# Performance work log

Hardware: AMD Instinct MI355X
Metric: run time of the kernel (lower is better)

Reference implementation:

```python
import jax, jax.numpy as jnp
import numpy as np

N_NODES = 50000


def setup_inputs() -> dict:
    key = jax.random.key(0)
    k1, k2, k3, k4 = jax.random.split(key, 4)
    in_c, hid = 256, 128
    x = jax.random.normal(k1, (N_NODES, in_c), dtype=jnp.float32)
    edge_index = jax.random.randint(k2, (2, 800000), 0, N_NODES, dtype=jnp.int32)
    # GCNConv weight (glorot) and bias
    W_conv = jax.random.normal(k3, (in_c, hid), dtype=jnp.float32) * (1.0 / np.sqrt(in_c))
    b_conv = jnp.zeros((hid,), dtype=jnp.float32)
    # Final Linear (xavier_uniform per reset_parameters)
    limit = np.sqrt(6.0 / (hid + in_c))
    W_lin = jax.random.uniform(k4, (hid, in_c), dtype=jnp.float32, minval=-limit, maxval=limit)
    b_lin = jnp.zeros((in_c,), dtype=jnp.float32)
    return {"x": x, "edge_index": edge_index, "W_conv": W_conv, "b_conv": b_conv,
            "W_lin": W_lin, "b_lin": b_lin}


def _gcn_conv(x, edge_index, W, b):
    n = x.shape[0]
    # add self-loops (standard GCN normalization)
    loop = jnp.arange(n, dtype=edge_index.dtype)
    src = jnp.concatenate([edge_index[0], loop])
    dst = jnp.concatenate([edge_index[1], loop])
    # transform first (in_c -> hid) so the edge gather moves the smaller dim
    h = x @ W  # [N, hid]
    deg = jax.ops.segment_sum(jnp.ones_like(dst, dtype=h.dtype), dst, num_segments=n)
    dinv = jnp.where(deg > 0, jax.lax.rsqrt(deg), 0.0)
    norm = dinv[src] * dinv[dst]  # [E+N]
    msg = h[src] * norm[:, None]  # [E+N, hid]
    out = jax.ops.segment_sum(msg, dst, num_segments=n)
    return out + b


def reference(x, edge_index, W_conv, b_conv, W_lin, b_lin):
    h = _gcn_conv(x, edge_index, W_conv, b_conv)  # [N, hid]
    # dropout p=0.0 -> identity
    return h @ W_lin + b_lin  # [N, in_c]
```

## Files before the change

kernel.cpp:

```cpp
#include <hip/hip_runtime.h>
#include <hip/hip_fp16.h>


#define N_NODES 50000
#define N_EDGES 800000
#define IN_C 256
#define HID 128
#define SCAN_BLOCKS ((N_NODES + 255) / 256)
#define GEMM_MBLK ((N_NODES + 63) / 64)

#define OFF_H    0UL
#define OFF_CONV 12800000UL
#define OFF_DEG  25600000UL
#define OFF_RP   25800000UL
#define OFF_DINV 26000064UL
#define OFF_RANK 26200064UL
#define OFF_REC  27800064UL
#define OFF_BSUM 31000064UL
#define OFF_WT1  31001088UL
#define OFF_WT2  31066624UL

typedef __attribute__((ext_vector_type(8))) short bf16x8;
typedef __attribute__((ext_vector_type(4))) float f32x4;

__device__ __forceinline__ ushort f2bf(float x) {
    unsigned u = __float_as_uint(x);
    u += 0x7fffu + ((u >> 16) & 1u);
    return (ushort)(u >> 16);
}

__global__ void deg_kernel(const int* __restrict__ dst, int* __restrict__ deg,
                           ushort* __restrict__ rank, int e) {
    int i = blockIdx.x * blockDim.x + threadIdx.x;
    if (i < e) rank[i] = (ushort)atomicAdd(&deg[dst[i]], 1);
}

__global__ __launch_bounds__(256) void scan_blocks_kernel(
    const int* __restrict__ deg, int* __restrict__ row_ptr,
    int* __restrict__ bsums, int n)
{
    __shared__ int tmp[256];
    int tid = threadIdx.x;
    int i = blockIdx.x * 256 + tid;
    int v = (i < n) ? deg[i] : 0;
    int orig = v;
    tmp[tid] = v;
    __syncthreads();
    #pragma unroll
    for (int off = 1; off < 256; off <<= 1) {
        int t = (tid >= off) ? tmp[tid - off] : 0;
        __syncthreads();
        tmp[tid] += t;
        __syncthreads();
    }
    if (i < n) row_ptr[i] = tmp[tid] - orig;
    if (tid == 255) bsums[blockIdx.x] = tmp[255];
}

__global__ __launch_bounds__(256) void scan_sums_kernel(int* __restrict__ bsums, int nb) {
    __shared__ int tmp[256];
    int tid = threadIdx.x;
    int v = (tid < nb) ? bsums[tid] : 0;
    int orig = v;
    tmp[tid] = v;
    __syncthreads();
    #pragma unroll
    for (int off = 1; off < 256; off <<= 1) {
        int t = (tid >= off) ? tmp[tid - off] : 0;
        __syncthreads();
        tmp[tid] += t;
        __syncthreads();
    }
    if (tid < nb) bsums[tid] = tmp[tid] - orig;
}

__global__ __launch_bounds__(256) void finalize_kernel(
    const int* __restrict__ deg, int* __restrict__ row_ptr,
    const int* __restrict__ bsums, float* __restrict__ dinv, int n)
{
    int i = blockIdx.x * 256 + threadIdx.x;
    if (i < n) {
        row_ptr[i] += bsums[blockIdx.x];
        dinv[i] = rsqrtf((float)(deg[i] + 1));
    }
    if (i == 0) row_ptr[n] = N_EDGES;
}

#define BUCKET_BLOCKS 2048
__global__ __launch_bounds__(256) void bucket_kernel(
    const int* __restrict__ src, const int* __restrict__ dst,
    const ushort* __restrict__ rank, const int* __restrict__ row_ptr,
    const float* __restrict__ dinv, unsigned* __restrict__ rec)
{
    int cls = blockIdx.x & 7;
    int blk = blockIdx.x >> 3;
    int lo = cls * (N_NODES / 8);
    int hi = lo + (N_NODES / 8);
    const int CHUNK = (N_EDGES + 255) / 256;
    int e0 = blk * CHUNK;
    int e1 = min(e0 + CHUNK, N_EDGES);
    for (int i = e0 + threadIdx.x; i < e1; i += 256) {
        int d = dst[i];
        if (d >= lo && d < hi) {
            int s = src[i];
            unsigned r = (unsigned)(ushort)s |
                         ((unsigned)__half_as_ushort(__float2half_rn(dinv[s])) << 16);
            rec[row_ptr[d] + rank[i]] = r;
        }
    }
}

__global__ void transpose_w_kernel(const float* __restrict__ W, ushort* __restrict__ Wt,
                                   int K, int N) {
    int i = blockIdx.x * 256 + threadIdx.x;
    if (i < N * K) {
        int n = i / K, k = i % K;
        Wt[i] = f2bf(W[k * N + n]);
    }
}

template <bool A_IS_BF16, bool BF16OUT>
__global__ __launch_bounds__(256) void mfma_gemm_kernel(
    const void* __restrict__ Av, const ushort* __restrict__ Bt,
    const float* __restrict__ bias, void* __restrict__ Cv,
    int M, int N, int K)
{
    constexpr int LDK = 40;
    __shared__ ushort As[64 * LDK];
    __shared__ ushort Bs[128 * LDK];
    int tid = threadIdx.x;
    int wave = tid >> 6, lane = tid & 63;
    int quad = lane >> 4, l16 = lane & 15;
    int wm0 = (wave >> 1) * 32, wn0 = (wave & 1) * 64;
    int bm = blockIdx.x * 64, bn = blockIdx.y * 128;

    f32x4 acc[2][4] = {};

    for (int k0 = 0; k0 < K; k0 += 32) {
        {
            int row = tid >> 2, col = (tid & 3) * 8;
            int grow = bm + row;
            if (A_IS_BF16) {
                bf16x8 v = {};
                if (grow < M)
                    v = *(const bf16x8*)((const ushort*)Av + (size_t)grow * K + k0 + col);
                *(bf16x8*)&As[row * LDK + col] = v;
            } else {
                float4 v0 = make_float4(0.f, 0.f, 0.f, 0.f);
                float4 v1 = make_float4(0.f, 0.f, 0.f, 0.f);
                if (grow < M) {
                    const float* ap = (const float*)Av + (size_t)grow * K + k0 + col;
                    v0 = *(const float4*)ap;
                    v1 = *(const float4*)(ap + 4);
                }
                ushort t[8] = {f2bf(v0.x), f2bf(v0.y), f2bf(v0.z), f2bf(v0.w),
                               f2bf(v1.x), f2bf(v1.y), f2bf(v1.z), f2bf(v1.w)};
                *(bf16x8*)&As[row * LDK + col] = *(bf16x8*)t;
            }
        }
        {
            int ch = tid * 2;
            int n = ch >> 2;
            int kk = (ch & 3) * 8;
            const ushort* bp = Bt + (size_t)(bn + n) * K + k0 + kk;
            *(bf16x8*)&Bs[n * LDK + kk]     = *(const bf16x8*)bp;
            *(bf16x8*)&Bs[n * LDK + kk + 8] = *(const bf16x8*)(bp + 8);
        }
        __syncthreads();
        bf16x8 af[2], bfr[4];
        #pragma unroll
        for (int im = 0; im < 2; ++im)
            af[im] = *(bf16x8*)&As[(wm0 + im * 16 + l16) * LDK + quad * 8];
        #pragma unroll
        for (int in = 0; in < 4; ++in)
            bfr[in] = *(bf16x8*)&Bs[(wn0 + in * 16 + l16) * LDK + quad * 8];
        #pragma unroll
        for (int im = 0; im < 2; ++im)
            #pragma unroll
            for (int in = 0; in < 4; ++in)
                acc[im][in] = __builtin_amdgcn_mfma_f32_16x16x32_bf16(
                    af[im], bfr[in], acc[im][in], 0, 0, 0);
        __syncthreads();
    }
    #pragma unroll
    for (int im = 0; im < 2; ++im) {
        #pragma unroll
        for (int in = 0; in < 4; ++in) {
            int col = bn + wn0 + in * 16 + l16;
            float bval = bias ? bias[col] : 0.f;
            #pragma unroll
            for (int r = 0; r < 4; ++r) {
                int grow = bm + wm0 + im * 16 + quad * 4 + r;
                if (grow < M) {
                    float o = acc[im][in][r] + bval;
                    if (BF16OUT)
                        ((ushort*)Cv)[(size_t)grow * N + col] = f2bf(o);
                    else
                        ((float*)Cv)[(size_t)grow * N + col] = o;
                }
            }
        }
    }
}

__global__ __launch_bounds__(256) void gather_kernel(
    const ushort* __restrict__ hb, const int* __restrict__ row_ptr,
    const unsigned* __restrict__ rec, const float* __restrict__ dinv,
    const float* __restrict__ b_conv, ushort* __restrict__ convb, int n)
{
    int wave = threadIdx.x >> 6;
    int lane = threadIdx.x & 63;
    int d = blockIdx.x * 4 + wave;
    if (d >= n) return;
    int c = lane << 1;
    float di = dinv[d];
    unsigned hv = *(const unsigned*)&hb[(size_t)d * HID + c];
    float2 acc;
    acc.x = di * __uint_as_float(hv << 16);
    acc.y = di * __uint_as_float(hv & 0xffff0000u);
    int begin = row_ptr[d], end = row_ptr[d + 1];
    int e = begin;
    for (; e + 4 <= end; e += 4) {
        unsigned r0 = rec[e], r1 = rec[e + 1], r2 = rec[e + 2], r3 = rec[e + 3];
        unsigned s0 = r0 & 0xffffu, s1 = r1 & 0xffffu, s2 = r2 & 0xffffu, s3 = r3 & 0xffffu;
        float w0 = __half2float(__ushort_as_half((ushort)(r0 >> 16)));
        float w1 = __half2float(__ushort_as_half((ushort)(r1 >> 16)));
        float w2 = __half2float(__ushort_as_half((ushort)(r2 >> 16)));
        float w3 = __half2float(__ushort_as_half((ushort)(r3 >> 16)));
        unsigned v0 = *(const unsigned*)&hb[(size_t)s0 * HID + c];
        unsigned v1 = *(const unsigned*)&hb[(size_t)s1 * HID + c];
        unsigned v2 = *(const unsigned*)&hb[(size_t)s2 * HID + c];
        unsigned v3 = *(const unsigned*)&hb[(size_t)s3 * HID + c];
        acc.x += w0 * __uint_as_float(v0 << 16);
        acc.y += w0 * __uint_as_float(v0 & 0xffff0000u);
        acc.x += w1 * __uint_as_float(v1 << 16);
        acc.y += w1 * __uint_as_float(v1 & 0xffff0000u);
        acc.x += w2 * __uint_as_float(v2 << 16);
        acc.y += w2 * __uint_as_float(v2 & 0xffff0000u);
        acc.x += w3 * __uint_as_float(v3 << 16);
        acc.y += w3 * __uint_as_float(v3 & 0xffff0000u);
    }
    for (; e < end; ++e) {
        unsigned r0 = rec[e];
        unsigned s0 = r0 & 0xffffu;
        float w0 = __half2float(__ushort_as_half((ushort)(r0 >> 16)));
        unsigned v0 = *(const unsigned*)&hb[(size_t)s0 * HID + c];
        acc.x += w0 * __uint_as_float(v0 << 16);
        acc.y += w0 * __uint_as_float(v0 & 0xffff0000u);
    }
    float ox = di * acc.x + b_conv[c];
    float oy = di * acc.y + b_conv[c + 1];
    unsigned po = ((unsigned)f2bf(oy) << 16) | (unsigned)f2bf(ox);
    *(unsigned*)&convb[(size_t)d * HID + c] = po;
}

extern "C" void kernel_launch(void* const* d_in, const int* in_sizes, int n_in,
                              void* d_out, int out_size, void* d_ws, size_t ws_size,
                              hipStream_t stream) {
    const float* x      = (const float*)d_in[0];
    const int*   ei     = (const int*)d_in[1];
    const float* W_conv = (const float*)d_in[2];
    const float* b_conv = (const float*)d_in[3];
    const float* W_lin  = (const float*)d_in[4];
    const float* b_lin  = (const float*)d_in[5];
    float* out = (float*)d_out;

    char* ws = (char*)d_ws;
    ushort* hb      = (ushort*)(ws + OFF_H);
    ushort* convb   = (ushort*)(ws + OFF_CONV);
    int*    deg     = (int*)(ws + OFF_DEG);
    int*    row_ptr = (int*)(ws + OFF_RP);
    float*  dinv    = (float*)(ws + OFF_DINV);
    ushort* rank    = (ushort*)(ws + OFF_RANK);
    unsigned* rec   = (unsigned*)(ws + OFF_REC);
    int*    bsums   = (int*)(ws + OFF_BSUM);
    ushort* wt_conv = (ushort*)(ws + OFF_WT1);
    ushort* wt_lin  = (ushort*)(ws + OFF_WT2);

    const int* src = ei;
    const int* dst = ei + N_EDGES;

    hipMemsetAsync(deg, 0, 200000, stream);

    deg_kernel<<<(N_EDGES + 255) / 256, 256, 0, stream>>>(dst, deg, rank, N_EDGES);
    scan_blocks_kernel<<<SCAN_BLOCKS, 256, 0, stream>>>(deg, row_ptr, bsums, N_NODES);
    scan_sums_kernel<<<1, 256, 0, stream>>>(bsums, SCAN_BLOCKS);
    finalize_kernel<<<SCAN_BLOCKS, 256, 0, stream>>>(deg, row_ptr, bsums, dinv, N_NODES);
    bucket_kernel<<<BUCKET_BLOCKS, 256, 0, stream>>>(src, dst, rank, row_ptr, dinv, rec);

    transpose_w_kernel<<<(HID * IN_C + 255) / 256, 256, 0, stream>>>(W_conv, wt_conv, IN_C, HID);
    transpose_w_kernel<<<(IN_C * HID + 255) / 256, 256, 0, stream>>>(W_lin, wt_lin, HID, IN_C);

    mfma_gemm_kernel<false, true><<<dim3(GEMM_MBLK, HID / 128), 256, 0, stream>>>(
        x, wt_conv, nullptr, hb, N_NODES, HID, IN_C);

    gather_kernel<<<(N_NODES + 3) / 4, 256, 0, stream>>>(
        hb, row_ptr, rec, dinv, b_conv, convb, N_NODES);

    mfma_gemm_kernel<true, false><<<dim3(GEMM_MBLK, IN_C / 128), 256, 0, stream>>>(
        convb, wt_lin, b_lin, out, N_NODES, IN_C, HID);
}
```

Before: 238.8 us.

## Vectorize gather, shrink rank to bytes, fuse scan and transpose launches

```diff
diff --git a/kernel.cpp b/kernel.cpp
--- a/kernel.cpp
+++ b/kernel.cpp
@@ -15,13 +15,14 @@
 #define OFF_RP   25800000UL
 #define OFF_DINV 26000064UL
 #define OFF_RANK 26200064UL
-#define OFF_REC  27800064UL
-#define OFF_BSUM 31000064UL
-#define OFF_WT1  31001088UL
-#define OFF_WT2  31066624UL
+#define OFF_REC  27000064UL
+#define OFF_BSUM 30200064UL
+#define OFF_WT1  30201088UL
+#define OFF_WT2  30266624UL
 
 typedef __attribute__((ext_vector_type(8))) short bf16x8;
 typedef __attribute__((ext_vector_type(4))) float f32x4;
+typedef unsigned char uchar;
 
 __device__ __forceinline__ ushort f2bf(float x) {
     unsigned u = __float_as_uint(x);
@@ -30,9 +31,9 @@
 }
 
 __global__ void deg_kernel(const int* __restrict__ dst, int* __restrict__ deg,
-                           ushort* __restrict__ rank, int e) {
+                           uchar* __restrict__ rank, int e) {
     int i = blockIdx.x * blockDim.x + threadIdx.x;
-    if (i < e) rank[i] = (ushort)atomicAdd(&deg[dst[i]], 1);
+    if (i < e) rank[i] = (uchar)atomicAdd(&deg[dst[i]], 1);
 }
 
 __global__ __launch_bounds__(256) void scan_blocks_kernel(
@@ -57,65 +58,68 @@
     if (tid == 255) bsums[blockIdx.x] = tmp[255];
 }
 
-__global__ __launch_bounds__(256) void scan_sums_kernel(int* __restrict__ bsums, int nb) {
-    __shared__ int tmp[256];
+__global__ __launch_bounds__(256) void finalize_kernel(
+    const int* __restrict__ deg, int* __restrict__ row_ptr,
+    const int* __restrict__ bsums, float* __restrict__ dinv, int n, int nb)
+{
+    __shared__ int red[256];
     int tid = threadIdx.x;
-    int v = (tid < nb) ? bsums[tid] : 0;
-    int orig = v;
-    tmp[tid] = v;
+    red[tid] = (tid < nb && tid < (int)blockIdx.x) ? bsums[tid] : 0;
     __syncthreads();
     #pragma unroll
-    for (int off = 1; off < 256; off <<= 1) {
-        int t = (tid >= off) ? tmp[tid - off] : 0;
-        __syncthreads();
-        tmp[tid] += t;
-        __syncthreads();
-    }
-    if (tid < nb) bsums[tid] = tmp[tid] - orig;
-}
-
-__global__ __launch_bounds__(256) void finalize_kernel(
-    const int* __restrict__ deg, int* __restrict__ row_ptr,
-    const int* __restrict__ bsums, float* __restrict__ dinv, int n)
-{
-    int i = blockIdx.x * 256 + threadIdx.x;
+    for (int off = 128; off > 0; off >>= 1) {
+        if (tid < off) red[tid] += red[tid + off];
+        __syncthreads();
+    }
+    int offset = red[0];
+    int i = blockIdx.x * 256 + tid;
     if (i < n) {
-        row_ptr[i] += bsums[blockIdx.x];
+        row_ptr[i] += offset;
         dinv[i] = rsqrtf((float)(deg[i] + 1));
     }
     if (i == 0) row_ptr[n] = N_EDGES;
 }
 
 #define BUCKET_BLOCKS 2048
+#define BUCKET_CHUNK 3128
 __global__ __launch_bounds__(256) void bucket_kernel(
     const int* __restrict__ src, const int* __restrict__ dst,
-    const ushort* __restrict__ rank, const int* __restrict__ row_ptr,
+    const uchar* __restrict__ rank, const int* __restrict__ row_ptr,
     const float* __restrict__ dinv, unsigned* __restrict__ rec)
 {
     int cls = blockIdx.x & 7;
     int blk = blockIdx.x >> 3;
     int lo = cls * (N_NODES / 8);
     int hi = lo + (N_NODES / 8);
-    const int CHUNK = (N_EDGES + 255) / 256;
-    int e0 = blk * CHUNK;
-    int e1 = min(e0 + CHUNK, N_EDGES);
-    for (int i = e0 + threadIdx.x; i < e1; i += 256) {
-        int d = dst[i];
-        if (d >= lo && d < hi) {
-            int s = src[i];
-            unsigned r = (unsigned)(ushort)s |
-                         ((unsigned)__half_as_ushort(__float2half_rn(dinv[s])) << 16);
-            rec[row_ptr[d] + rank[i]] = r;
+    int e0 = blk * BUCKET_CHUNK;
+    int e1 = min(e0 + BUCKET_CHUNK, N_EDGES);
+    for (int i = e0 + threadIdx.x * 4; i < e1; i += 1024) {
+        int4 d4 = *(const int4*)&dst[i];
+        #pragma unroll
+        for (int k = 0; k < 4; ++k) {
+            int d = (k == 0) ? d4.x : (k == 1) ? d4.y : (k == 2) ? d4.z : d4.w;
+            if (d >= lo && d < hi) {
+                int s = src[i + k];
+                unsigned r = (unsigned)(ushort)s |
+                             ((unsigned)__half_as_ushort(__float2half_rn(dinv[s])) << 16);
+                rec[row_ptr[d] + rank[i + k]] = r;
+            }
         }
     }
 }
 
-__global__ void transpose_w_kernel(const float* __restrict__ W, ushort* __restrict__ Wt,
-                                   int K, int N) {
+__global__ void transpose_w_kernel(const float* __restrict__ W_conv,
+                                   const float* __restrict__ W_lin,
+                                   ushort* __restrict__ wt_conv,
+                                   ushort* __restrict__ wt_lin) {
     int i = blockIdx.x * 256 + threadIdx.x;
-    if (i < N * K) {
-        int n = i / K, k = i % K;
-        Wt[i] = f2bf(W[k * N + n]);
+    if (i < HID * IN_C) {
+        int nn = i / IN_C, k = i % IN_C;
+        wt_conv[i] = f2bf(W_conv[k * HID + nn]);
+    } else {
+        int j = i - HID * IN_C;
+        int nn = j / HID, k = j % HID;
+        wt_lin[j] = f2bf(W_lin[k * IN_C + nn]);
     }
 }
 
@@ -203,6 +207,21 @@
     }
 }
 
+__device__ __forceinline__ void acc_edge(float4& a0, float4& a1, unsigned r,
+                                         const ushort* __restrict__ hb, int c) {
+    unsigned s = r & 0xffffu;
+    float w = __half2float(__ushort_as_half((ushort)(r >> 16)));
+    uint4 v = *(const uint4*)&hb[(size_t)s * HID + c];
+    a0.x += w * __uint_as_float(v.x << 16);
+    a0.y += w * __uint_as_float(v.x & 0xffff0000u);
+    a0.z += w * __uint_as_float(v.y << 16);
+    a0.w += w * __uint_as_float(v.y & 0xffff0000u);
+    a1.x += w * __uint_as_float(v.z << 16);
+    a1.y += w * __uint_as_float(v.z & 0xffff0000u);
+    a1.z += w * __uint_as_float(v.w << 16);
+    a1.w += w * __uint_as_float(v.w & 0xffff0000u);
+}
+
 __global__ __launch_bounds__(256) void gather_kernel(
     const ushort* __restrict__ hb, const int* __restrict__ row_ptr,
     const unsigned* __restrict__ rec, const float* __restrict__ dinv,
@@ -212,46 +231,56 @@
     int lane = threadIdx.x & 63;
     int d = blockIdx.x * 4 + wave;
     if (d >= n) return;
-    int c = lane << 1;
-    float di = dinv[d];
-    unsigned hv = *(const unsigned*)&hb[(size_t)d * HID + c];
-    float2 acc;
-    acc.x = di * __uint_as_float(hv << 16);
-    acc.y = di * __uint_as_float(hv & 0xffff0000u);
+    int grp = lane >> 4;
+    int l16 = lane & 15;
+    int c = l16 << 3;
+
+    float4 a0 = make_float4(0.f, 0.f, 0.f, 0.f);
+    float4 a1 = make_float4(0.f, 0.f, 0.f, 0.f);
     int begin = row_ptr[d], end = row_ptr[d + 1];
-    int e = begin;
-    for (; e + 4 <= end; e += 4) {
-        unsigned r0 = rec[e], r1 = rec[e + 1], r2 = rec[e + 2], r3 = rec[e + 3];
-        unsigned s0 = r0 & 0xffffu, s1 = r1 & 0xffffu, s2 = r2 & 0xffffu, s3 = r3 & 0xffffu;
-        float w0 = __half2float(__ushort_as_half((ushort)(r0 >> 16)));
-        float w1 = __half2float(__ushort_as_half((ushort)(r1 >> 16)));
-        float w2 = __half2float(__ushort_as_half((ushort)(r2 >> 16)));
-        float w3 = __half2float(__ushort_as_half((ushort)(r3 >> 16)));
-        unsigned v0 = *(const unsigned*)&hb[(size_t)s0 * HID + c];
-        unsigned v1 = *(const unsigned*)&hb[(size_t)s1 * HID + c];
-        unsigned v2 = *(const unsigned*)&hb[(size_t)s2 * HID + c];
-        unsigned v3 = *(const unsigned*)&hb[(size_t)s3 * HID + c];
-        acc.x += w0 * __uint_as_float(v0 << 16);
-        acc.y += w0 * __uint_as_float(v0 & 0xffff0000u);
-        acc.x += w1 * __uint_as_float(v1 << 16);
-        acc.y += w1 * __uint_as_float(v1 & 0xffff0000u);
-        acc.x += w2 * __uint_as_float(v2 << 16);
-        acc.y += w2 * __uint_as_float(v2 & 0xffff0000u);
-        acc.x += w3 * __uint_as_float(v3 << 16);
-        acc.y += w3 * __uint_as_float(v3 & 0xffff0000u);
-    }
-    for (; e < end; ++e) {
+    int e = begin + grp;
+    for (; e + 12 < end; e += 16) {
         unsigned r0 = rec[e];
-        unsigned s0 = r0 & 0xffffu;
-        float w0 = __half2float(__ushort_as_half((ushort)(r0 >> 16)));
-        unsigned v0 = *(const unsigned*)&hb[(size_t)s0 * HID + c];
-        acc.x += w0 * __uint_as_float(v0 << 16);
-        acc.y += w0 * __uint_as_float(v0 & 0xffff0000u);
-    }
-    float ox = di * acc.x + b_conv[c];
-    float oy = di * acc.y + b_conv[c + 1];
-    unsigned po = ((unsigned)f2bf(oy) << 16) | (unsigned)f2bf(ox);
-    *(unsigned*)&convb[(size_t)d * HID + c] = po;
+        unsigned r1 = rec[e + 4];
+        unsigned r2 = rec[e + 8];
+        unsigned r3 = rec[e + 12];
+        acc_edge(a0, a1, r0, hb, c);
+        acc_edge(a0, a1, r1, hb, c);
+        acc_edge(a0, a1, r2, hb, c);
+        acc_edge(a0, a1, r3, hb, c);
+    }
+    for (; e < end; e += 4)
+        acc_edge(a0, a1, rec[e], hb, c);
+
+    a0.x += __shfl_xor(a0.x, 16); a0.y += __shfl_xor(a0.y, 16);
+    a0.z += __shfl_xor(a0.z, 16); a0.w += __shfl_xor(a0.w, 16);
+    a1.x += __shfl_xor(a1.x, 16); a1.y += __shfl_xor(a1.y, 16);
+    a1.z += __shfl_xor(a1.z, 16); a1.w += __shfl_xor(a1.w, 16);
+    a0.x += __shfl_xor(a0.x, 32); a0.y += __shfl_xor(a0.y, 32);
+    a0.z += __shfl_xor(a0.z, 32); a0.w += __shfl_xor(a0.w, 32);
+    a1.x += __shfl_xor(a1.x, 32); a1.y += __shfl_xor(a1.y, 32);
+    a1.z += __shfl_xor(a1.z, 32); a1.w += __shfl_xor(a1.w, 32);
+
+    if (grp == 0) {
+        float di = dinv[d];
+        uint4 hv = *(const uint4*)&hb[(size_t)d * HID + c];
+        a0.x += di * __uint_as_float(hv.x << 16);
+        a0.y += di * __uint_as_float(hv.x & 0xffff0000u);
+        a0.z += di * __uint_as_float(hv.y << 16);
+        a0.w += di * __uint_as_float(hv.y & 0xffff0000u);
+        a1.x += di * __uint_as_float(hv.z << 16);
+        a1.y += di * __uint_as_float(hv.z & 0xffff0000u);
+        a1.z += di * __uint_as_float(hv.w << 16);
+        a1.w += di * __uint_as_float(hv.w & 0xffff0000u);
+        float4 b0 = *(const float4*)&b_conv[c];
+        float4 b1 = *(const float4*)&b_conv[c + 4];
+        uint4 po;
+        po.x = ((unsigned)f2bf(di * a0.y + b0.y) << 16) | (unsigned)f2bf(di * a0.x + b0.x);
+        po.y = ((unsigned)f2bf(di * a0.w + b0.w) << 16) | (unsigned)f2bf(di * a0.z + b0.z);
+        po.z = ((unsigned)f2bf(di * a1.y + b1.y) << 16) | (unsigned)f2bf(di * a1.x + b1.x);
+        po.w = ((unsigned)f2bf(di * a1.w + b1.w) << 16) | (unsigned)f2bf(di * a1.z + b1.z);
+        *(uint4*)&convb[(size_t)d * HID + c] = po;
+    }
 }
 
 extern "C" void kernel_launch(void* const* d_in, const int* in_sizes, int n_in,
@@ -271,7 +300,7 @@
     int*    deg     = (int*)(ws + OFF_DEG);
     int*    row_ptr = (int*)(ws + OFF_RP);
     float*  dinv    = (float*)(ws + OFF_DINV);
-    ushort* rank    = (ushort*)(ws + OFF_RANK);
+    uchar*  rank    = (uchar*)(ws + OFF_RANK);
     unsigned* rec   = (unsigned*)(ws + OFF_REC);
     int*    bsums   = (int*)(ws + OFF_BSUM);
     ushort* wt_conv = (ushort*)(ws + OFF_WT1);
@@ -284,12 +313,12 @@
 
     deg_kernel<<<(N_EDGES + 255) / 256, 256, 0, stream>>>(dst, deg, rank, N_EDGES);
     scan_blocks_kernel<<<SCAN_BLOCKS, 256, 0, stream>>>(deg, row_ptr, bsums, N_NODES);
-    scan_sums_kernel<<<1, 256, 0, stream>>>(bsums, SCAN_BLOCKS);
-    finalize_kernel<<<SCAN_BLOCKS, 256, 0, stream>>>(deg, row_ptr, bsums, dinv, N_NODES);
+    finalize_kernel<<<SCAN_BLOCKS, 256, 0, stream>>>(deg, row_ptr, bsums, dinv,
+                                                     N_NODES, SCAN_BLOCKS);
     bucket_kernel<<<BUCKET_BLOCKS, 256, 0, stream>>>(src, dst, rank, row_ptr, dinv, rec);
 
-    transpose_w_kernel<<<(HID * IN_C + 255) / 256, 256, 0, stream>>>(W_conv, wt_conv, IN_C, HID);
-    transpose_w_kernel<<<(IN_C * HID + 255) / 256, 256, 0, stream>>>(W_lin, wt_lin, HID, IN_C);
+    transpose_w_kernel<<<(HID * IN_C * 2 + 255) / 256, 256, 0, stream>>>(
+        W_conv, W_lin, wt_conv, wt_lin);
 
     mfma_gemm_kernel<false, true><<<dim3(GEMM_MBLK, HID / 128), 256, 0, stream>>>(
         x, wt_conv, nullptr, hb, N_NODES, HID, IN_C);
```

Measured after the change: 233.0 us. 2.4% less time.
